# Kernel optimization log

Hardware: AMD Instinct MI355X
Metric: run time of the kernel (lower is better)

Reference implementation:

```python
import jax, jax.numpy as jnp
import numpy as np
from jax import lax

TOP_K = 4
N_GROUP = 4
TOPK_GROUP = 2
ROUTED_SCALING = 2.5
NORM_TOPK = True


def relu2(v):
    r = jax.nn.relu(v)
    return r * r


def setup_inputs() -> dict:
    key = jax.random.key(0)
    ks = jax.random.split(key, 7)
    B, S, H, E, I, IS = 2, 2048, 1024, 16, 512, 2048
    x = jax.random.normal(ks[0], (B, S, H), dtype=jnp.float32)
    router_w = jax.random.normal(ks[1], (E, H), dtype=jnp.float32) * 0.02
    bias = jnp.zeros((E,), dtype=jnp.float32)
    w_up = jax.random.normal(ks[2], (E, I, H), dtype=jnp.float32) * 0.02
    w_down = jax.random.normal(ks[3], (E, H, I), dtype=jnp.float32) * 0.02
    ws_up = jax.random.normal(ks[4], (IS, H), dtype=jnp.float32) * 0.02
    ws_down = jax.random.normal(ks[5], (H, IS), dtype=jnp.float32) * 0.02
    return {"x": x, "router_w": router_w, "bias": bias, "w_up": w_up,
            "w_down": w_down, "ws_up": ws_up, "ws_down": ws_down,
            "attn_metadata": 0}


def _route(xf, router_w, bias):
    # xf: [T, H] float32
    T = xf.shape[0]
    E = router_w.shape[0]
    logits = xf @ router_w.T                      # [T, E]
    scores = jax.nn.sigmoid(logits)
    sfc = scores + bias[None, :]                  # scores_for_choice
    # group scores: sum of top-2 within each group
    g = sfc.reshape(T, N_GROUP, E // N_GROUP)
    group_scores = lax.top_k(g, 2)[0].sum(-1)     # [T, G]
    _, gidx = lax.top_k(group_scores, TOPK_GROUP)
    gmask = jax.nn.one_hot(gidx, N_GROUP, dtype=sfc.dtype).sum(1)  # [T, G]
    smask = jnp.repeat(gmask, E // N_GROUP, axis=1)                # [T, E]
    masked = jnp.where(smask > 0, sfc, 0.0)
    _, tidx = lax.top_k(masked, TOP_K)            # [T, K]
    tw = jnp.take_along_axis(scores, tidx, axis=1)
    if NORM_TOPK:
        tw = tw / (tw.sum(-1, keepdims=True) + 1e-20)
    tw = tw * ROUTED_SCALING
    return tidx, tw


def reference(x, router_w, bias, w_up, w_down, ws_up, ws_down, attn_metadata):
    B, S, H = x.shape
    E = w_up.shape[0]
    xf = x.reshape(-1, H).astype(jnp.float32)     # [T, H]
    tidx, tw = _route(xf, router_w, bias)
    # combine weights per (token, expert): scatter-add topk weights
    T = xf.shape[0]
    comb = jnp.zeros((T, E), dtype=tw.dtype).at[jnp.arange(T)[:, None], tidx].add(tw)
    # routed experts (dense grouped form; zero combine weight == not routed)
    up = jnp.einsum('th,eih->tei', xf, w_up)      # [T, E, I]
    h = relu2(up) * comb[:, :, None]
    routed = jnp.einsum('tei,ehi->th', h, w_down) # [T, H]
    routed = routed.reshape(B, S, H).astype(x.dtype)
    # shared expert on residual
    shared = relu2(jnp.einsum('bsh,ih->bsi', x, ws_up))
    shared = jnp.einsum('bsi,hi->bsh', shared, ws_down)
    return routed + shared
```

## Files before the change

### kernel.cpp

```cpp
#include <hip/hip_runtime.h>
#include <stdint.h>

#define T_TOK 4096
#define H_DIM 1024
#define E_NUM 16
#define I_DIM 512
#define IS_DIM 2048
#define TOPK 4
#define NGRP 4
#define GSZ 4
#define MAXMT 32
#define NCHUNK 64

#define S0 1048576
#define S1 1572864
#define S2 2097152
#define S3 4194304
#define S4 6291456

typedef unsigned short u16;
typedef __attribute__((ext_vector_type(8))) short short8;
typedef __attribute__((ext_vector_type(4))) float f32x4;

__device__ __forceinline__ void gload16(const void* g, void* l) {
  __builtin_amdgcn_global_load_lds(
      (const __attribute__((address_space(1))) void*)g,
      (__attribute__((address_space(3))) void*)l, 16, 0, 0);
}

__device__ __forceinline__ u16 f2bf(float f) {
  union { float f; uint32_t u; } v; v.f = f;
  uint32_t u = v.u;
  uint32_t r = (u + 0x7fffu + ((u >> 16) & 1u)) >> 16;
  return (u16)r;
}

__device__ __forceinline__ float bf2f(u16 h) {
  union { uint32_t u; float f; } v; v.u = ((uint32_t)h) << 16;
  return v.f;
}

__global__ __launch_bounds__(256) void cvt_all_kernel(
    const float* __restrict__ x, const float* __restrict__ wsu,
    const float* __restrict__ wsd, const float* __restrict__ wu,
    const float* __restrict__ wd,
    u16* __restrict__ xb, u16* __restrict__ wsub, u16* __restrict__ wsdb,
    u16* __restrict__ wub, u16* __restrict__ wdb) {
  int i = blockIdx.x * 256 + threadIdx.x;
  const float4* src; ushort4* dst; int base;
  if (i < S0)      { src = (const float4*)x;   dst = (ushort4*)xb;   base = 0;  }
  else if (i < S1) { src = (const float4*)wsu; dst = (ushort4*)wsub; base = S0; }
  else if (i < S2) { src = (const float4*)wsd; dst = (ushort4*)wsdb; base = S1; }
  else if (i < S3) { src = (const float4*)wu;  dst = (ushort4*)wub;  base = S2; }
  else             { src = (const float4*)wd;  dst = (ushort4*)wdb;  base = S3; }
  float4 v = src[i - base];
  ushort4 o;
  o.x = f2bf(v.x); o.y = f2bf(v.y); o.z = f2bf(v.z); o.w = f2bf(v.w);
  dst[i - base] = o;
}

__global__ __launch_bounds__(256) void route_kernel(
    const float* __restrict__ x, const float* __restrict__ rw,
    const float* __restrict__ bias, int* __restrict__ tidx_out,
    float* __restrict__ tw_out) {
  const int wave = threadIdx.x >> 6;
  const int lane = threadIdx.x & 63;
  const int t = blockIdx.x * 4 + wave;

  const float4* xr = reinterpret_cast<const float4*>(x + (size_t)t * H_DIM);
  const float4* rw4 = reinterpret_cast<const float4*>(rw);
  float4 xv[4];
#pragma unroll
  for (int j = 0; j < 4; ++j) xv[j] = xr[lane + j * 64];

  double acc[E_NUM];
#pragma unroll
  for (int e = 0; e < E_NUM; ++e) {
    double a = 0.0;
#pragma unroll
    for (int j = 0; j < 4; ++j) {
      float4 w = rw4[e * 256 + lane + j * 64];
      a += (double)xv[j].x * (double)w.x;
      a += (double)xv[j].y * (double)w.y;
      a += (double)xv[j].z * (double)w.z;
      a += (double)xv[j].w * (double)w.w;
    }
    acc[e] = a;
  }
#pragma unroll
  for (int e = 0; e < E_NUM; ++e) {
#pragma unroll
    for (int off = 32; off; off >>= 1) acc[e] += __shfl_xor(acc[e], off);
  }
  if (lane == 0) {
    float scores[E_NUM], sfc[E_NUM];
#pragma unroll
    for (int e = 0; e < E_NUM; ++e) {
      scores[e] = 1.0f / (1.0f + expf((float)(-acc[e])));
      sfc[e] = scores[e] + bias[e];
    }
    float gs[NGRP];
#pragma unroll
    for (int g = 0; g < NGRP; ++g) {
      float m1 = -1e30f, m2 = -1e30f;
#pragma unroll
      for (int j = 0; j < GSZ; ++j) {
        float v = sfc[g * GSZ + j];
        if (v > m1) { m2 = m1; m1 = v; } else if (v > m2) { m2 = v; }
      }
      gs[g] = m1 + m2;
    }
    int g1 = 0;
    for (int g = 1; g < NGRP; ++g) if (gs[g] > gs[g1]) g1 = g;
    int g2 = -1;
    for (int g = 0; g < NGRP; ++g) {
      if (g == g1) continue;
      if (g2 < 0 || gs[g] > gs[g2]) g2 = g;
    }
    float masked[E_NUM];
#pragma unroll
    for (int e = 0; e < E_NUM; ++e) {
      int g = e / GSZ;
      masked[e] = (g == g1 || g == g2) ? sfc[e] : 0.0f;
    }
    int tidx[TOPK]; float tw[TOPK];
#pragma unroll
    for (int k = 0; k < TOPK; ++k) {
      int best = 0; float bv = masked[0];
      for (int e = 1; e < E_NUM; ++e)
        if (masked[e] > bv) { bv = masked[e]; best = e; }
      tidx[k] = best; tw[k] = scores[best]; masked[best] = -1e30f;
    }
    float s = tw[0] + tw[1] + tw[2] + tw[3] + 1e-20f;
#pragma unroll
    for (int k = 0; k < TOPK; ++k) {
      tidx_out[t * TOPK + k] = tidx[k];
      tw_out[t * TOPK + k] = tw[k] / s * 2.5f;
    }
  }
}

__global__ __launch_bounds__(256) void hist_kernel(const int* __restrict__ tidx,
                                                   int* __restrict__ partial) {
  const int c = blockIdx.x;
  const int tid = threadIdx.x;
  const int lane = tid & 63;
  const int w = tid >> 6;
  __shared__ int h[4][E_NUM];
  const int e = tidx[c * 256 + tid];
#pragma unroll
  for (int ee = 0; ee < E_NUM; ++ee) {
    unsigned long long b = __ballot(e == ee);
    if (lane == 0) h[w][ee] = __popcll(b);
  }
  __syncthreads();
  if (tid < E_NUM)
    partial[c * E_NUM + tid] = h[0][tid] + h[1][tid] + h[2][tid] + h[3][tid];
}

__global__ __launch_bounds__(256) void prefix2_kernel(
    const int* __restrict__ partial, int* __restrict__ chunk_base,
    int* __restrict__ counts, int* __restrict__ offsets) {
  __shared__ int tot[E_NUM];
  __shared__ int offs[E_NUM];
  const int tid = threadIdx.x;
  if (tid < E_NUM) {
    int run = 0;
    for (int c = 0; c < NCHUNK; ++c) {
      chunk_base[c * E_NUM + tid] = run;
      run += partial[c * E_NUM + tid];
    }
    tot[tid] = run;
    counts[tid] = run;
  }
  __syncthreads();
  if (tid == 0) {
    int s = 0;
    for (int e = 0; e < E_NUM; ++e) { offs[e] = s; offsets[e] = s; s += tot[e]; }
    offsets[E_NUM] = s;
  }
  __syncthreads();
  for (int i = tid; i < NCHUNK * E_NUM; i += 256)
    chunk_base[i] += offs[i & 15];
}

__global__ __launch_bounds__(256) void scatter2_kernel(
    const int* __restrict__ tidx, const float* __restrict__ tw,
    const int* __restrict__ chunk_base,
    int* __restrict__ tok_g, float* __restrict__ w_g, int* __restrict__ pos_map) {
  const int c = blockIdx.x;
  const int tid = threadIdx.x;
  const int lane = tid & 63;
  const int w = tid >> 6;
  __shared__ int h[4][E_NUM];
  const int i = c * 256 + tid;
  const int e = tidx[i];
  int pre = 0;
#pragma unroll
  for (int ee = 0; ee < E_NUM; ++ee) {
    unsigned long long b = __ballot(e == ee);
    if (lane == 0) h[w][ee] = __popcll(b);
    if (ee == e) pre = __popcll(b & ((1ull << lane) - 1ull));
  }
  __syncthreads();
  int rank = pre;
  for (int ww = 0; ww < w; ++ww) rank += h[ww][e];
  const int pos = chunk_base[c * E_NUM + e] + rank;
  tok_g[pos] = i >> 2;
  w_g[pos] = tw[i];
  pos_map[i] = pos;
}

template <int EPI>
__global__ __launch_bounds__(256, 3) void gemm_bt(
    const u16* __restrict__ Abase, const u16* __restrict__ Bbase,
    float* __restrict__ Cf, u16* __restrict__ Cb,
    int M, int N, int K,
    const int* __restrict__ counts, const int* __restrict__ offsets,
    const int* __restrict__ tok_g, const float* __restrict__ w_g,
    const int* __restrict__ pos_map, const u16* __restrict__ Rd) {
  __shared__ __align__(16) u16 As[2][128 * 64];
  __shared__ __align__(16) u16 Bs[2][64 * 64];

  const int cpx = gridDim.x >> 3;
  const int wg = (blockIdx.x & 7) * cpx + (blockIdx.x >> 3);

  const int NT = N >> 6;
  int mt, nt, cnt = M, obase = 0;
  const u16* A = Abase;
  const u16* B = Bbase;

  if constexpr (EPI <= 1) {
    mt = wg / NT;
    nt = wg - mt * NT;
  } else {
    const int per_e = MAXMT * NT;
    int e = wg / per_e;
    int r = wg - e * per_e;
    mt = r / NT;
    nt = r - mt * NT;
    cnt = counts[e];
    if (mt * 128 >= cnt) return;
    obase = offsets[e];
    if constexpr (EPI == 2) {
      B = Bbase + (size_t)e * (I_DIM * H_DIM);
    } else {
      A = Abase + (size_t)obase * I_DIM;
      B = Bbase + (size_t)e * (H_DIM * I_DIM);
    }
  }

  const int tid = threadIdx.x;
  const int srow = tid >> 3;
  const int slot = tid & 7;
  const u16* gA[4];
  const u16* gB[2];
#pragma unroll
  for (int p = 0; p < 4; ++p) {
    int rloc = p * 32 + srow;
    int ks = ((slot ^ (rloc & 7)) << 3);
    int am = mt * 128 + rloc;
    if constexpr (EPI == 2) {
      int tk = tok_g[obase + ((am < cnt) ? am : 0)];
      gA[p] = Abase + (size_t)tk * H_DIM + ks;
    } else if constexpr (EPI == 3) {
      gA[p] = A + (size_t)((am < cnt) ? am : 0) * K + ks;
    } else {
      gA[p] = A + (size_t)am * K + ks;
    }
  }
#pragma unroll
  for (int p = 0; p < 2; ++p) {
    int rloc = p * 32 + srow;
    int ks = ((slot ^ (rloc & 7)) << 3);
    gB[p] = B + (size_t)(nt * 64 + rloc) * K + ks;
  }

  const int wave = tid >> 6;
  const int lane = tid & 63;
  const int wr = wave >> 1;
  const int wc = wave & 1;
  const int frow = lane & 15;
  const int l4 = lane >> 4;

  int a_off[4][2], b_off[2][2];
#pragma unroll
  for (int m = 0; m < 4; ++m) {
    int row = wr * 64 + m * 16 + frow;
#pragma unroll
    for (int kk = 0; kk < 2; ++kk)
      a_off[m][kk] = (row << 6) + ((((kk << 2) + l4) ^ (row & 7)) << 3);
  }
#pragma unroll
  for (int n = 0; n < 2; ++n) {
    int row = wc * 32 + n * 16 + frow;
#pragma unroll
    for (int kk = 0; kk < 2; ++kk)
      b_off[n][kk] = (row << 6) + ((((kk << 2) + l4) ^ (row & 7)) << 3);
  }

  f32x4 acc[4][2];
#pragma unroll
  for (int m = 0; m < 4; ++m)
#pragma unroll
    for (int n = 0; n < 2; ++n) acc[m][n] = (f32x4)0.0f;

  const int dst = tid << 3;
  auto stage = [&](int k0, int c) {
#pragma unroll
    for (int p = 0; p < 4; ++p)
      gload16(gA[p] + k0, &As[c][(p << 11) + dst]);
#pragma unroll
    for (int p = 0; p < 2; ++p)
      gload16(gB[p] + k0, &Bs[c][(p << 11) + dst]);
  };

  const int KT = K >> 6;
  stage(0, 0);
  int cur = 0;
  for (int kt = 0; kt < KT; ++kt) {
    __syncthreads();
    if (kt + 1 < KT) stage((kt + 1) << 6, cur ^ 1);
#pragma unroll
    for (int kk = 0; kk < 2; ++kk) {
      short8 a[4], b[2];
#pragma unroll
      for (int m = 0; m < 4; ++m)
        a[m] = *reinterpret_cast<const short8*>(&As[cur][a_off[m][kk]]);
#pragma unroll
      for (int n = 0; n < 2; ++n)
        b[n] = *reinterpret_cast<const short8*>(&Bs[cur][b_off[n][kk]]);
      __builtin_amdgcn_s_setprio(1);
#pragma unroll
      for (int m = 0; m < 4; ++m)
#pragma unroll
        for (int n = 0; n < 2; ++n)
          acc[m][n] = __builtin_amdgcn_mfma_f32_16x16x32_bf16(a[m], b[n], acc[m][n], 0, 0, 0);
      __builtin_amdgcn_s_setprio(0);
    }
    cur ^= 1;
  }

  const int rbase = l4 << 2;
  const int cbase = frow;
#pragma unroll
  for (int m = 0; m < 4; ++m) {
#pragma unroll
    for (int r = 0; r < 4; ++r) {
      int lr = wr * 64 + (m << 4) + rbase + r;
      int grow = mt * 128 + lr;
      if (EPI >= 2 && grow >= cnt) continue;
      float wv = 1.0f;
      if constexpr (EPI == 2) wv = w_g[obase + grow];
      const int* pm = nullptr;
      if constexpr (EPI == 1) pm = pos_map + grow * TOPK;
#pragma unroll
      for (int n = 0; n < 2; ++n) {
        int gc = nt * 64 + wc * 32 + (n << 4) + cbase;
        float v = acc[m][n][r];
        if constexpr (EPI == 0) {
          float tpos = fmaxf(v, 0.0f);
          Cb[(size_t)grow * N + gc] = f2bf(tpos * tpos);
        } else if constexpr (EPI == 1) {
          v += bf2f(Rd[(size_t)pm[0] * H_DIM + gc]);
          v += bf2f(Rd[(size_t)pm[1] * H_DIM + gc]);
          v += bf2f(Rd[(size_t)pm[2] * H_DIM + gc]);
          v += bf2f(Rd[(size_t)pm[3] * H_DIM + gc]);
          Cf[(size_t)grow * N + gc] = v;
        } else if constexpr (EPI == 2) {
          float tpos = fmaxf(v, 0.0f);
          Cb[(size_t)(obase + grow) * I_DIM + gc] = f2bf(tpos * tpos * wv);
        } else {
          Cb[(size_t)(obase + grow) * N + gc] = f2bf(v);
        }
      }
    }
  }
}

extern "C" void kernel_launch(void* const* d_in, const int* in_sizes, int n_in,
                              void* d_out, int out_size, void* d_ws, size_t ws_size,
                              hipStream_t stream) {
  const float* x = (const float*)d_in[0];
  const float* rw = (const float*)d_in[1];
  const float* bias = (const float*)d_in[2];
  const float* w_up = (const float*)d_in[3];
  const float* w_down = (const float*)d_in[4];
  const float* ws_up = (const float*)d_in[5];
  const float* ws_down = (const float*)d_in[6];
  float* out = (float*)d_out;

  uint8_t* wsb = (uint8_t*)d_ws;
  size_t off = 0;
  auto alloc = [&](size_t bytes) {
    void* p = wsb + off;
    off += (bytes + 255) & ~(size_t)255;
    return p;
  };
  u16* x_bf = (u16*)alloc((size_t)T_TOK * H_DIM * 2);
  u16* wsup_bf = (u16*)alloc((size_t)IS_DIM * H_DIM * 2);
  u16* wsdn_bf = (u16*)alloc((size_t)H_DIM * IS_DIM * 2);
  u16* wup_bf = (u16*)alloc((size_t)E_NUM * I_DIM * H_DIM * 2);
  u16* wdn_bf = (u16*)alloc((size_t)E_NUM * H_DIM * I_DIM * 2);
  u16* hs = (u16*)alloc((size_t)T_TOK * IS_DIM * 2);
  u16* hp = (u16*)alloc((size_t)(T_TOK * TOPK + 128) * I_DIM * 2);
  u16* hp_down = (u16*)alloc((size_t)(T_TOK * TOPK + 128) * H_DIM * 2);
  int* counts = (int*)alloc(64);
  int* offsets = (int*)alloc(128);
  int* tok_g = (int*)alloc((size_t)(T_TOK * TOPK) * 4);
  float* w_g = (float*)alloc((size_t)(T_TOK * TOPK) * 4);
  int* pos_map = (int*)alloc((size_t)(T_TOK * TOPK) * 4);
  int* tidx_buf = (int*)alloc((size_t)T_TOK * TOPK * 4);
  float* tw_buf = (float*)alloc((size_t)T_TOK * TOPK * 4);
  int* partial = (int*)alloc((size_t)NCHUNK * E_NUM * 4);
  int* chunk_base = (int*)alloc((size_t)NCHUNK * E_NUM * 4);

  cvt_all_kernel<<<S4 / 256, 256, 0, stream>>>(
      x, ws_up, ws_down, w_up, w_down,
      x_bf, wsup_bf, wsdn_bf, wup_bf, wdn_bf);

  route_kernel<<<T_TOK / 4, 256, 0, stream>>>(x, rw, bias, tidx_buf, tw_buf);
  hist_kernel<<<NCHUNK, 256, 0, stream>>>(tidx_buf, partial);
  prefix2_kernel<<<1, 256, 0, stream>>>(partial, chunk_base, counts, offsets);
  scatter2_kernel<<<NCHUNK, 256, 0, stream>>>(tidx_buf, tw_buf, chunk_base,
                                              tok_g, w_g, pos_map);

  gemm_bt<0><<<(T_TOK / 128) * (IS_DIM / 64), 256, 0, stream>>>(
      x_bf, wsup_bf, nullptr, hs, T_TOK, IS_DIM, H_DIM,
      nullptr, nullptr, nullptr, nullptr, nullptr, nullptr);
  gemm_bt<2><<<E_NUM * MAXMT * (I_DIM / 64), 256, 0, stream>>>(
      x_bf, wup_bf, nullptr, hp, T_TOK, I_DIM, H_DIM,
      counts, offsets, tok_g, w_g, nullptr, nullptr);
  gemm_bt<3><<<E_NUM * MAXMT * (H_DIM / 64), 256, 0, stream>>>(
      hp, wdn_bf, nullptr, hp_down, T_TOK, H_DIM, I_DIM,
      counts, offsets, tok_g, w_g, nullptr, nullptr);
  gemm_bt<1><<<(T_TOK / 128) * (H_DIM / 64), 256, 0, stream>>>(
      hs, wsdn_bf, out, nullptr, T_TOK, H_DIM, IS_DIM,
      nullptr, nullptr, nullptr, nullptr, pos_map, hp_down);
}
```

Baseline: 194.8 us.

## Fuse bf16 weight conversion into GEMM B-tile loads and x conversion into routing

Drops the standalone conversion pass over all inputs. Activations are now converted to bf16 inside the routing kernel, and the fp32 weights are read directly by each GEMM, packed to bf16 in registers with v_cvt_pk_bf16_f32, and stored to LDS. This removes a full read and write of all weight tensors per call. In exchange, each GEMM tile re-reads fp32 weights (twice the bytes) and the B loads go through registers instead of the async global-to-LDS path, which adds register pressure and latency to the pipeline.

```diff
diff --git a/kernel.cpp b/kernel.cpp
--- a/kernel.cpp
+++ b/kernel.cpp
@@ -12,12 +12,6 @@
 #define MAXMT 32
 #define NCHUNK 64
 
-#define S0 1048576
-#define S1 1572864
-#define S2 2097152
-#define S3 4194304
-#define S4 6291456
-
 typedef unsigned short u16;
 typedef __attribute__((ext_vector_type(8))) short short8;
 typedef __attribute__((ext_vector_type(4))) float f32x4;
@@ -40,38 +34,33 @@
   return v.f;
 }
 
-__global__ __launch_bounds__(256) void cvt_all_kernel(
-    const float* __restrict__ x, const float* __restrict__ wsu,
-    const float* __restrict__ wsd, const float* __restrict__ wu,
-    const float* __restrict__ wd,
-    u16* __restrict__ xb, u16* __restrict__ wsub, u16* __restrict__ wsdb,
-    u16* __restrict__ wub, u16* __restrict__ wdb) {
-  int i = blockIdx.x * 256 + threadIdx.x;
-  const float4* src; ushort4* dst; int base;
-  if (i < S0)      { src = (const float4*)x;   dst = (ushort4*)xb;   base = 0;  }
-  else if (i < S1) { src = (const float4*)wsu; dst = (ushort4*)wsub; base = S0; }
-  else if (i < S2) { src = (const float4*)wsd; dst = (ushort4*)wsdb; base = S1; }
-  else if (i < S3) { src = (const float4*)wu;  dst = (ushort4*)wub;  base = S2; }
-  else             { src = (const float4*)wd;  dst = (ushort4*)wdb;  base = S3; }
-  float4 v = src[i - base];
-  ushort4 o;
-  o.x = f2bf(v.x); o.y = f2bf(v.y); o.z = f2bf(v.z); o.w = f2bf(v.w);
-  dst[i - base] = o;
+__device__ __forceinline__ uint32_t cvtpk(float lo, float hi) {
+  uint32_t r;
+  asm volatile("v_cvt_pk_bf16_f32 %0, %1, %2" : "=v"(r) : "v"(lo), "v"(hi));
+  return r;
 }
 
 __global__ __launch_bounds__(256) void route_kernel(
     const float* __restrict__ x, const float* __restrict__ rw,
     const float* __restrict__ bias, int* __restrict__ tidx_out,
-    float* __restrict__ tw_out) {
+    float* __restrict__ tw_out, u16* __restrict__ x_bf) {
   const int wave = threadIdx.x >> 6;
   const int lane = threadIdx.x & 63;
   const int t = blockIdx.x * 4 + wave;
 
   const float4* xr = reinterpret_cast<const float4*>(x + (size_t)t * H_DIM);
   const float4* rw4 = reinterpret_cast<const float4*>(rw);
+  ushort4* xbw = reinterpret_cast<ushort4*>(x_bf + (size_t)t * H_DIM);
   float4 xv[4];
 #pragma unroll
   for (int j = 0; j < 4; ++j) xv[j] = xr[lane + j * 64];
+#pragma unroll
+  for (int j = 0; j < 4; ++j) {
+    ushort4 o;
+    o.x = f2bf(xv[j].x); o.y = f2bf(xv[j].y);
+    o.z = f2bf(xv[j].z); o.w = f2bf(xv[j].w);
+    xbw[lane + j * 64] = o;
+  }
 
   double acc[E_NUM];
 #pragma unroll
@@ -213,7 +202,7 @@
 
 template <int EPI>
 __global__ __launch_bounds__(256, 3) void gemm_bt(
-    const u16* __restrict__ Abase, const u16* __restrict__ Bbase,
+    const u16* __restrict__ Abase, const float* __restrict__ Bbase,
     float* __restrict__ Cf, u16* __restrict__ Cb,
     int M, int N, int K,
     const int* __restrict__ counts, const int* __restrict__ offsets,
@@ -228,7 +217,7 @@
   const int NT = N >> 6;
   int mt, nt, cnt = M, obase = 0;
   const u16* A = Abase;
-  const u16* B = Bbase;
+  const float* B = Bbase;
 
   if constexpr (EPI <= 1) {
     mt = wg / NT;
@@ -254,7 +243,6 @@
   const int srow = tid >> 3;
   const int slot = tid & 7;
   const u16* gA[4];
-  const u16* gB[2];
 #pragma unroll
   for (int p = 0; p < 4; ++p) {
     int rloc = p * 32 + srow;
@@ -269,11 +257,12 @@
       gA[p] = A + (size_t)am * K + ks;
     }
   }
+  const float* gBf[2];
 #pragma unroll
   for (int p = 0; p < 2; ++p) {
     int rloc = p * 32 + srow;
     int ks = ((slot ^ (rloc & 7)) << 3);
-    gB[p] = B + (size_t)(nt * 64 + rloc) * K + ks;
+    gBf[p] = B + (size_t)(nt * 64 + rloc) * K + ks;
   }
 
   const int wave = tid >> 6;
@@ -306,21 +295,42 @@
     for (int n = 0; n < 2; ++n) acc[m][n] = (f32x4)0.0f;
 
   const int dst = tid << 3;
-  auto stage = [&](int k0, int c) {
+  auto stageA = [&](int k0, int c) {
 #pragma unroll
     for (int p = 0; p < 4; ++p)
       gload16(gA[p] + k0, &As[c][(p << 11) + dst]);
-#pragma unroll
-    for (int p = 0; p < 2; ++p)
-      gload16(gB[p] + k0, &Bs[c][(p << 11) + dst]);
   };
+  float4 bl[2][2];
+  auto issueB = [&](int k0) {
+#pragma unroll
+    for (int p = 0; p < 2; ++p) {
+      bl[p][0] = *reinterpret_cast<const float4*>(gBf[p] + k0);
+      bl[p][1] = *reinterpret_cast<const float4*>(gBf[p] + k0 + 4);
+    }
+  };
+  auto writeB = [&](int c) {
+#pragma unroll
+    for (int p = 0; p < 2; ++p) {
+      uint4 q;
+      q.x = cvtpk(bl[p][0].x, bl[p][0].y);
+      q.y = cvtpk(bl[p][0].z, bl[p][0].w);
+      q.z = cvtpk(bl[p][1].x, bl[p][1].y);
+      q.w = cvtpk(bl[p][1].z, bl[p][1].w);
+      *reinterpret_cast<uint4*>(&Bs[c][(p << 11) + dst]) = q;
+    }
+  };
 
   const int KT = K >> 6;
-  stage(0, 0);
+  issueB(0);
+  stageA(0, 0);
+  writeB(0);
   int cur = 0;
   for (int kt = 0; kt < KT; ++kt) {
     __syncthreads();
-    if (kt + 1 < KT) stage((kt + 1) << 6, cur ^ 1);
+    if (kt + 1 < KT) {
+      issueB((kt + 1) << 6);
+      stageA((kt + 1) << 6, cur ^ 1);
+    }
 #pragma unroll
     for (int kk = 0; kk < 2; ++kk) {
       short8 a[4], b[2];
@@ -338,6 +348,7 @@
           acc[m][n] = __builtin_amdgcn_mfma_f32_16x16x32_bf16(a[m], b[n], acc[m][n], 0, 0, 0);
       __builtin_amdgcn_s_setprio(0);
     }
+    if (kt + 1 < KT) writeB(cur ^ 1);
     cur ^= 1;
   }
 
@@ -398,10 +409,6 @@
     return p;
   };
   u16* x_bf = (u16*)alloc((size_t)T_TOK * H_DIM * 2);
-  u16* wsup_bf = (u16*)alloc((size_t)IS_DIM * H_DIM * 2);
-  u16* wsdn_bf = (u16*)alloc((size_t)H_DIM * IS_DIM * 2);
-  u16* wup_bf = (u16*)alloc((size_t)E_NUM * I_DIM * H_DIM * 2);
-  u16* wdn_bf = (u16*)alloc((size_t)E_NUM * H_DIM * I_DIM * 2);
   u16* hs = (u16*)alloc((size_t)T_TOK * IS_DIM * 2);
   u16* hp = (u16*)alloc((size_t)(T_TOK * TOPK + 128) * I_DIM * 2);
   u16* hp_down = (u16*)alloc((size_t)(T_TOK * TOPK + 128) * H_DIM * 2);
@@ -415,26 +422,22 @@
   int* partial = (int*)alloc((size_t)NCHUNK * E_NUM * 4);
   int* chunk_base = (int*)alloc((size_t)NCHUNK * E_NUM * 4);
 
-  cvt_all_kernel<<<S4 / 256, 256, 0, stream>>>(
-      x, ws_up, ws_down, w_up, w_down,
-      x_bf, wsup_bf, wsdn_bf, wup_bf, wdn_bf);
-
-  route_kernel<<<T_TOK / 4, 256, 0, stream>>>(x, rw, bias, tidx_buf, tw_buf);
+  route_kernel<<<T_TOK / 4, 256, 0, stream>>>(x, rw, bias, tidx_buf, tw_buf, x_bf);
   hist_kernel<<<NCHUNK, 256, 0, stream>>>(tidx_buf, partial);
   prefix2_kernel<<<1, 256, 0, stream>>>(partial, chunk_base, counts, offsets);
   scatter2_kernel<<<NCHUNK, 256, 0, stream>>>(tidx_buf, tw_buf, chunk_base,
                                               tok_g, w_g, pos_map);
 
   gemm_bt<0><<<(T_TOK / 128) * (IS_DIM / 64), 256, 0, stream>>>(
-      x_bf, wsup_bf, nullptr, hs, T_TOK, IS_DIM, H_DIM,
+      x_bf, ws_up, nullptr, hs, T_TOK, IS_DIM, H_DIM,
       nullptr, nullptr, nullptr, nullptr, nullptr, nullptr);
   gemm_bt<2><<<E_NUM * MAXMT * (I_DIM / 64), 256, 0, stream>>>(
-      x_bf, wup_bf, nullptr, hp, T_TOK, I_DIM, H_DIM,
+      x_bf, w_up, nullptr, hp, T_TOK, I_DIM, H_DIM,
       counts, offsets, tok_g, w_g, nullptr, nullptr);
   gemm_bt<3><<<E_NUM * MAXMT * (H_DIM / 64), 256, 0, stream>>>(
-      hp, wdn_bf, nullptr, hp_down, T_TOK, H_DIM, I_DIM,
+      hp, w_down, nullptr, hp_down, T_TOK, H_DIM, I_DIM,
       counts, offsets, tok_g, w_g, nullptr, nullptr);
   gemm_bt<1><<<(T_TOK / 128) * (H_DIM / 64), 256, 0, stream>>>(
-      hs, wsdn_bf, out, nullptr, T_TOK, H_DIM, IS_DIM,
+      hs, ws_down, out, nullptr, T_TOK, H_DIM, IS_DIM,
       nullptr, nullptr, nullptr, nullptr, pos_map, hp_down);
 }
```

New measurement: 243.4 us. 1.25x slower.

## Fuse x conversion into routing and merge shared and routed up-GEMMs

Applied to the files above, without the earlier changes.

The x fp32-to-bf16 conversion moves into the routing kernel, which already reads x, so that separate read pass is dropped. The shared-expert up-projection and the routed-expert up-projection become one launch, gemm_up, whose grid covers both tile sets, which should fill the GPU better and remove a kernel boundary. Weight conversion still runs in its own kernel, now after routing. The merged kernel uses runtime branches where the old code had template specialization, which may add register pressure or divergence.

```diff
diff --git a/kernel.cpp b/kernel.cpp
--- a/kernel.cpp
+++ b/kernel.cpp
@@ -12,11 +12,10 @@
 #define MAXMT 32
 #define NCHUNK 64
 
-#define S0 1048576
-#define S1 1572864
-#define S2 2097152
-#define S3 4194304
-#define S4 6291456
+#define W0 524288
+#define W1 1048576
+#define W2 3145728
+#define W3 5242880
 
 typedef unsigned short u16;
 typedef __attribute__((ext_vector_type(8))) short short8;
@@ -40,19 +39,17 @@
   return v.f;
 }
 
-__global__ __launch_bounds__(256) void cvt_all_kernel(
-    const float* __restrict__ x, const float* __restrict__ wsu,
-    const float* __restrict__ wsd, const float* __restrict__ wu,
-    const float* __restrict__ wd,
-    u16* __restrict__ xb, u16* __restrict__ wsub, u16* __restrict__ wsdb,
+__global__ __launch_bounds__(256) void cvt_w_kernel(
+    const float* __restrict__ wsu, const float* __restrict__ wsd,
+    const float* __restrict__ wu, const float* __restrict__ wd,
+    u16* __restrict__ wsub, u16* __restrict__ wsdb,
     u16* __restrict__ wub, u16* __restrict__ wdb) {
   int i = blockIdx.x * 256 + threadIdx.x;
   const float4* src; ushort4* dst; int base;
-  if (i < S0)      { src = (const float4*)x;   dst = (ushort4*)xb;   base = 0;  }
-  else if (i < S1) { src = (const float4*)wsu; dst = (ushort4*)wsub; base = S0; }
-  else if (i < S2) { src = (const float4*)wsd; dst = (ushort4*)wsdb; base = S1; }
-  else if (i < S3) { src = (const float4*)wu;  dst = (ushort4*)wub;  base = S2; }
-  else             { src = (const float4*)wd;  dst = (ushort4*)wdb;  base = S3; }
+  if (i < W0)      { src = (const float4*)wsu; dst = (ushort4*)wsub; base = 0;  }
+  else if (i < W1) { src = (const float4*)wsd; dst = (ushort4*)wsdb; base = W0; }
+  else if (i < W2) { src = (const float4*)wu;  dst = (ushort4*)wub;  base = W1; }
+  else             { src = (const float4*)wd;  dst = (ushort4*)wdb;  base = W2; }
   float4 v = src[i - base];
   ushort4 o;
   o.x = f2bf(v.x); o.y = f2bf(v.y); o.z = f2bf(v.z); o.w = f2bf(v.w);
@@ -62,16 +59,24 @@
 __global__ __launch_bounds__(256) void route_kernel(
     const float* __restrict__ x, const float* __restrict__ rw,
     const float* __restrict__ bias, int* __restrict__ tidx_out,
-    float* __restrict__ tw_out) {
+    float* __restrict__ tw_out, u16* __restrict__ x_bf) {
   const int wave = threadIdx.x >> 6;
   const int lane = threadIdx.x & 63;
   const int t = blockIdx.x * 4 + wave;
 
   const float4* xr = reinterpret_cast<const float4*>(x + (size_t)t * H_DIM);
   const float4* rw4 = reinterpret_cast<const float4*>(rw);
+  ushort4* xbw = reinterpret_cast<ushort4*>(x_bf + (size_t)t * H_DIM);
   float4 xv[4];
 #pragma unroll
   for (int j = 0; j < 4; ++j) xv[j] = xr[lane + j * 64];
+#pragma unroll
+  for (int j = 0; j < 4; ++j) {
+    ushort4 o;
+    o.x = f2bf(xv[j].x); o.y = f2bf(xv[j].y);
+    o.z = f2bf(xv[j].z); o.w = f2bf(xv[j].w);
+    xbw[lane + j * 64] = o;
+  }
 
   double acc[E_NUM];
 #pragma unroll
@@ -211,6 +216,153 @@
   pos_map[i] = pos;
 }
 
+#define NB_SH ((T_TOK / 128) * (IS_DIM / 64))
+#define NB_UP (NB_SH + E_NUM * MAXMT * (I_DIM / 64))
+__global__ __launch_bounds__(256, 3) void gemm_up(
+    const u16* __restrict__ x_bf, const u16* __restrict__ wsup_bf,
+    const u16* __restrict__ wup_bf, u16* __restrict__ hs, u16* __restrict__ hp,
+    const int* __restrict__ counts, const int* __restrict__ offsets,
+    const int* __restrict__ tok_g, const float* __restrict__ w_g) {
+  __shared__ __align__(16) u16 As[2][128 * 64];
+  __shared__ __align__(16) u16 Bs[2][64 * 64];
+
+  const int cpx = gridDim.x >> 3;
+  const int wg = (blockIdx.x & 7) * cpx + (blockIdx.x >> 3);
+
+  const bool shared = (wg < NB_SH);
+  int mt, nt, cnt, obase = 0, Nout;
+  const u16* B;
+  if (shared) {
+    mt = wg >> 5;
+    nt = wg & 31;
+    cnt = T_TOK;
+    Nout = IS_DIM;
+    B = wsup_bf;
+  } else {
+    int r = wg - NB_SH;
+    const int per_e = MAXMT * (I_DIM >> 6);
+    int e = r >> 8;
+    r &= 255;
+    mt = r >> 3;
+    nt = r & 7;
+    cnt = counts[e];
+    if (mt * 128 >= cnt) return;
+    obase = offsets[e];
+    Nout = I_DIM;
+    B = wup_bf + (size_t)e * (I_DIM * H_DIM);
+  }
+  const int K = H_DIM;
+
+  const int tid = threadIdx.x;
+  const int srow = tid >> 3;
+  const int slot = tid & 7;
+  const u16* gA[4];
+#pragma unroll
+  for (int p = 0; p < 4; ++p) {
+    int rloc = p * 32 + srow;
+    int ks = ((slot ^ (rloc & 7)) << 3);
+    int am = mt * 128 + rloc;
+    int row;
+    if (shared) row = am;
+    else row = tok_g[obase + ((am < cnt) ? am : 0)];
+    gA[p] = x_bf + (size_t)row * H_DIM + ks;
+  }
+  const u16* gB[2];
+#pragma unroll
+  for (int p = 0; p < 2; ++p) {
+    int rloc = p * 32 + srow;
+    int ks = ((slot ^ (rloc & 7)) << 3);
+    gB[p] = B + (size_t)(nt * 64 + rloc) * K + ks;
+  }
+
+  const int wave = tid >> 6;
+  const int lane = tid & 63;
+  const int wr = wave >> 1;
+  const int wc = wave & 1;
+  const int frow = lane & 15;
+  const int l4 = lane >> 4;
+
+  int a_off[4][2], b_off[2][2];
+#pragma unroll
+  for (int m = 0; m < 4; ++m) {
+    int row = wr * 64 + m * 16 + frow;
+#pragma unroll
+    for (int kk = 0; kk < 2; ++kk)
+      a_off[m][kk] = (row << 6) + ((((kk << 2) + l4) ^ (row & 7)) << 3);
+  }
+#pragma unroll
+  for (int n = 0; n < 2; ++n) {
+    int row = wc * 32 + n * 16 + frow;
+#pragma unroll
+    for (int kk = 0; kk < 2; ++kk)
+      b_off[n][kk] = (row << 6) + ((((kk << 2) + l4) ^ (row & 7)) << 3);
+  }
+
+  f32x4 acc[4][2];
+#pragma unroll
+  for (int m = 0; m < 4; ++m)
+#pragma unroll
+    for (int n = 0; n < 2; ++n) acc[m][n] = (f32x4)0.0f;
+
+  const int dst = tid << 3;
+  auto stage = [&](int k0, int c) {
+#pragma unroll
+    for (int p = 0; p < 4; ++p)
+      gload16(gA[p] + k0, &As[c][(p << 11) + dst]);
+#pragma unroll
+    for (int p = 0; p < 2; ++p)
+      gload16(gB[p] + k0, &Bs[c][(p << 11) + dst]);
+  };
+
+  const int KT = K >> 6;
+  stage(0, 0);
+  int cur = 0;
+  for (int kt = 0; kt < KT; ++kt) {
+    __syncthreads();
+    if (kt + 1 < KT) stage((kt + 1) << 6, cur ^ 1);
+#pragma unroll
+    for (int kk = 0; kk < 2; ++kk) {
+      short8 a[4], b[2];
+#pragma unroll
+      for (int m = 0; m < 4; ++m)
+        a[m] = *reinterpret_cast<const short8*>(&As[cur][a_off[m][kk]]);
+#pragma unroll
+      for (int n = 0; n < 2; ++n)
+        b[n] = *reinterpret_cast<const short8*>(&Bs[cur][b_off[n][kk]]);
+      __builtin_amdgcn_s_setprio(1);
+#pragma unroll
+      for (int m = 0; m < 4; ++m)
+#pragma unroll
+        for (int n = 0; n < 2; ++n)
+          acc[m][n] = __builtin_amdgcn_mfma_f32_16x16x32_bf16(a[m], b[n], acc[m][n], 0, 0, 0);
+      __builtin_amdgcn_s_setprio(0);
+    }
+    cur ^= 1;
+  }
+
+  const int rbase = l4 << 2;
+  const int cbase = frow;
+#pragma unroll
+  for (int m = 0; m < 4; ++m) {
+#pragma unroll
+    for (int r = 0; r < 4; ++r) {
+      int lr = wr * 64 + (m << 4) + rbase + r;
+      int grow = mt * 128 + lr;
+      if (!shared && grow >= cnt) continue;
+      float wv = shared ? 1.0f : w_g[obase + grow];
+#pragma unroll
+      for (int n = 0; n < 2; ++n) {
+        int gc = nt * 64 + wc * 32 + (n << 4) + cbase;
+        float v = acc[m][n][r];
+        float tpos = fmaxf(v, 0.0f);
+        float o = tpos * tpos * wv;
+        if (shared) hs[(size_t)grow * IS_DIM + gc] = f2bf(o);
+        else hp[(size_t)(obase + grow) * I_DIM + gc] = f2bf(o);
+      }
+    }
+  }
+}
+
 template <int EPI>
 __global__ __launch_bounds__(256, 3) void gemm_bt(
     const u16* __restrict__ Abase, const u16* __restrict__ Bbase,
@@ -230,7 +382,7 @@
   const u16* A = Abase;
   const u16* B = Bbase;
 
-  if constexpr (EPI <= 1) {
+  if constexpr (EPI == 1) {
     mt = wg / NT;
     nt = wg - mt * NT;
   } else {
@@ -242,33 +394,26 @@
     cnt = counts[e];
     if (mt * 128 >= cnt) return;
     obase = offsets[e];
-    if constexpr (EPI == 2) {
-      B = Bbase + (size_t)e * (I_DIM * H_DIM);
-    } else {
-      A = Abase + (size_t)obase * I_DIM;
-      B = Bbase + (size_t)e * (H_DIM * I_DIM);
-    }
+    A = Abase + (size_t)obase * I_DIM;
+    B = Bbase + (size_t)e * (H_DIM * I_DIM);
   }
 
   const int tid = threadIdx.x;
   const int srow = tid >> 3;
   const int slot = tid & 7;
   const u16* gA[4];
-  const u16* gB[2];
 #pragma unroll
   for (int p = 0; p < 4; ++p) {
     int rloc = p * 32 + srow;
     int ks = ((slot ^ (rloc & 7)) << 3);
     int am = mt * 128 + rloc;
-    if constexpr (EPI == 2) {
-      int tk = tok_g[obase + ((am < cnt) ? am : 0)];
-      gA[p] = Abase + (size_t)tk * H_DIM + ks;
-    } else if constexpr (EPI == 3) {
+    if constexpr (EPI == 3) {
       gA[p] = A + (size_t)((am < cnt) ? am : 0) * K + ks;
     } else {
       gA[p] = A + (size_t)am * K + ks;
     }
   }
+  const u16* gB[2];
 #pragma unroll
   for (int p = 0; p < 2; ++p) {
     int rloc = p * 32 + srow;
@@ -349,27 +494,19 @@
     for (int r = 0; r < 4; ++r) {
       int lr = wr * 64 + (m << 4) + rbase + r;
       int grow = mt * 128 + lr;
-      if (EPI >= 2 && grow >= cnt) continue;
-      float wv = 1.0f;
-      if constexpr (EPI == 2) wv = w_g[obase + grow];
+      if (EPI == 3 && grow >= cnt) continue;
       const int* pm = nullptr;
       if constexpr (EPI == 1) pm = pos_map + grow * TOPK;
 #pragma unroll
       for (int n = 0; n < 2; ++n) {
         int gc = nt * 64 + wc * 32 + (n << 4) + cbase;
         float v = acc[m][n][r];
-        if constexpr (EPI == 0) {
-          float tpos = fmaxf(v, 0.0f);
-          Cb[(size_t)grow * N + gc] = f2bf(tpos * tpos);
-        } else if constexpr (EPI == 1) {
+        if constexpr (EPI == 1) {
           v += bf2f(Rd[(size_t)pm[0] * H_DIM + gc]);
           v += bf2f(Rd[(size_t)pm[1] * H_DIM + gc]);
           v += bf2f(Rd[(size_t)pm[2] * H_DIM + gc]);
           v += bf2f(Rd[(size_t)pm[3] * H_DIM + gc]);
           Cf[(size_t)grow * N + gc] = v;
-        } else if constexpr (EPI == 2) {
-          float tpos = fmaxf(v, 0.0f);
-          Cb[(size_t)(obase + grow) * I_DIM + gc] = f2bf(tpos * tpos * wv);
         } else {
           Cb[(size_t)(obase + grow) * N + gc] = f2bf(v);
         }
@@ -415,22 +552,16 @@
   int* partial = (int*)alloc((size_t)NCHUNK * E_NUM * 4);
   int* chunk_base = (int*)alloc((size_t)NCHUNK * E_NUM * 4);
 
-  cvt_all_kernel<<<S4 / 256, 256, 0, stream>>>(
-      x, ws_up, ws_down, w_up, w_down,
-      x_bf, wsup_bf, wsdn_bf, wup_bf, wdn_bf);
-
-  route_kernel<<<T_TOK / 4, 256, 0, stream>>>(x, rw, bias, tidx_buf, tw_buf);
+  route_kernel<<<T_TOK / 4, 256, 0, stream>>>(x, rw, bias, tidx_buf, tw_buf, x_bf);
   hist_kernel<<<NCHUNK, 256, 0, stream>>>(tidx_buf, partial);
   prefix2_kernel<<<1, 256, 0, stream>>>(partial, chunk_base, counts, offsets);
   scatter2_kernel<<<NCHUNK, 256, 0, stream>>>(tidx_buf, tw_buf, chunk_base,
                                               tok_g, w_g, pos_map);
-
-  gemm_bt<0><<<(T_TOK / 128) * (IS_DIM / 64), 256, 0, stream>>>(
-      x_bf, wsup_bf, nullptr, hs, T_TOK, IS_DIM, H_DIM,
-      nullptr, nullptr, nullptr, nullptr, nullptr, nullptr);
-  gemm_bt<2><<<E_NUM * MAXMT * (I_DIM / 64), 256, 0, stream>>>(
-      x_bf, wup_bf, nullptr, hp, T_TOK, I_DIM, H_DIM,
-      counts, offsets, tok_g, w_g, nullptr, nullptr);
+  cvt_w_kernel<<<W3 / 256, 256, 0, stream>>>(
+      ws_up, ws_down, w_up, w_down, wsup_bf, wsdn_bf, wup_bf, wdn_bf);
+
+  gemm_up<<<NB_UP, 256, 0, stream>>>(
+      x_bf, wsup_bf, wup_bf, hs, hp, counts, offsets, tok_g, w_g);
   gemm_bt<3><<<E_NUM * MAXMT * (H_DIM / 64), 256, 0, stream>>>(
       hp, wdn_bf, nullptr, hp_down, T_TOK, H_DIM, I_DIM,
       counts, offsets, tok_g, w_g, nullptr, nullptr);
```

After: 248.9 us. +27.8%, slower.
